# Kernel tuning notes

Measured on AMD Instinct MI355X. Metric: run time of the kernel, lower is better.

The kernel has to match this reference:

```python
import jax, jax.numpy as jnp
import numpy as np

B, F, T, D = 8, 256, 32, 1024
NEG = -1e30


def setup_inputs() -> dict:
    key = jax.random.key(0)
    ks = jax.random.split(key, 10)
    s = 1.0 / np.sqrt(D)
    return {
        "features": jax.random.normal(ks[0], (B, F, D), jnp.float32),
        "masks": jnp.ones((B, F), jnp.float32),  # unused by the module
        "textual_features": jax.random.normal(ks[1], (B, T, D), jnp.float32),
        "q_masks": jax.random.randint(ks[2], (B, T), 0, 2, jnp.int32),
        "Ws": jax.random.normal(ks[3], (D, D), jnp.float32) * s,
        "W": jax.random.normal(ks[4], (D, D), jnp.float32) * s,
        "w": jax.random.normal(ks[5], (D, 1), jnp.float32) * s,
        "b": jax.random.normal(ks[6], (1, D), jnp.float32) * s,
        "Wcw": jax.random.normal(ks[7], (1, D), jnp.float32) * s,
        "bcw": jnp.zeros((1,), jnp.float32),
        "Wcb": jax.random.normal(ks[8], (1, D), jnp.float32) * s,
        "bcb": jnp.zeros((1,), jnp.float32),
    }


def reference(features, masks, textual_features, q_masks, Ws, W, w, b, Wcw, bcw, Wcb, bcb):
    # Vectorized over all f_len frames at once (original loops over k).
    txt_proj = jnp.einsum("btd,de->bte", textual_features, Ws)   # [B,T,D]
    feat_proj = jnp.einsum("bfd,de->bfe", features, W)           # [B,F,D]
    # additive-attention hidden: [B,F,T,D]
    h = jnp.tanh(txt_proj[:, None, :, :] + feat_proj[:, :, None, :] + b[None, None, :, :][..., 0, :])
    rho = jnp.einsum("bftd,d->bft", h, w[:, 0])                  # [B,F,T]
    qm = q_masks.astype(jnp.float32)
    rho = rho + (1.0 - qm)[:, None, :] * NEG                     # mask_logits
    att = jax.nn.softmax(rho, axis=-1)                          # over t_len
    txt_h = jnp.einsum("bft,btd->bfd", att, textual_features)    # [B,F,D]
    w_s = jnp.tanh(jnp.einsum("bfd,od->bfo", txt_h, Wcw) + bcw)  # [B,F,1]
    b_s = jnp.tanh(jnp.einsum("bfd,od->bfo", txt_h, Wcb) + bcb)  # [B,F,1]
    return w_s * features + b_s
```

## Files before the change

### kernel.cpp

```cpp
#include <hip/hip_runtime.h>
#include <math.h>

#define Bdim 8
#define Fdim 256
#define Tdim 32
#define Ddim 1024
#define NEGV (-1e30f)
#define TANH_SCALE 2.8853900817779268f
#define LOG2E 1.4426950408889634f

typedef unsigned short ushort;
using short8  = __attribute__((ext_vector_type(8))) short;
using floatx4 = __attribute__((ext_vector_type(4))) float;

__device__ __forceinline__ float fexp2(float x) { return __builtin_amdgcn_exp2f(x); }
__device__ __forceinline__ float frcp(float x)  { return __builtin_amdgcn_rcpf(x); }

__device__ __forceinline__ float fast_tanh(float x) {
    return 1.0f - 2.0f * frcp(fexp2(x * TANH_SCALE) + 1.0f);
}

__device__ __forceinline__ ushort f2bf(float f) {
    unsigned u = __float_as_uint(f);
    unsigned r = u + 0x7FFFu + ((u >> 16) & 1u);
    return (ushort)(r >> 16);
}

__global__ __launch_bounds__(256) void prep(
    const float* __restrict__ feat, const float* __restrict__ txt,
    const float* __restrict__ W, const float* __restrict__ Ws,
    ushort* __restrict__ featB, ushort* __restrict__ txtB,
    ushort* __restrict__ WtB, ushort* __restrict__ WstB)
{
    __shared__ ushort tile[32][33];
    const int blk = blockIdx.x;
    const int NCAST = Bdim * Fdim + Bdim * Tdim;
    if (blk < NCAST) {
        const float* in; ushort* out; int base;
        if (blk < Bdim * Fdim) { in = feat; out = featB; base = blk * Ddim; }
        else { in = txt; out = txtB; base = (blk - Bdim * Fdim) * Ddim; }
        const int i = base + threadIdx.x * 4;
        float4 v = *(const float4*)(in + i);
        ushort4 o;
        o.x = f2bf(v.x); o.y = f2bf(v.y); o.z = f2bf(v.z); o.w = f2bf(v.w);
        *(ushort4*)(out + i) = o;
    } else {
        int t = blk - NCAST;
        const float* in = (t < 1024) ? W : Ws;
        ushort* out = (t < 1024) ? WtB : WstB;
        t &= 1023;
        const int bx = (t & 31) * 32;
        const int by = (t >> 5) * 32;
        const int tx = threadIdx.x & 31;
        const int tg = threadIdx.x >> 5;
        #pragma unroll
        for (int r = tg; r < 32; r += 8)
            tile[r][tx] = f2bf(in[(size_t)(by + r) * Ddim + bx + tx]);
        __syncthreads();
        #pragma unroll
        for (int r = tg; r < 32; r += 8)
            out[(size_t)(bx + r) * Ddim + by + tx] = tile[tx][r];
    }
}

#define GBK 32

__device__ __forceinline__ int swz(int row, int kUsh) {
    int ch = (kUsh >> 3) ^ ((row >> 1) & 3);
    return row * GBK + ch * 8 + (kUsh & 7);
}

__global__ __launch_bounds__(256) void gemm_dual(
    const ushort* __restrict__ A1, const ushort* __restrict__ Bt1, float* __restrict__ C1,
    const ushort* __restrict__ A2, const ushort* __restrict__ Bt2, float* __restrict__ C2,
    const float* __restrict__ bias2)
{
    const int K = Ddim, N = Ddim;
    const int by = blockIdx.y;
    const ushort* A; const ushort* Bt; float* C; const float* bias; int m0;
    if (by < 32) { A = A1; Bt = Bt1; C = C1; bias = nullptr; m0 = by * 64; }
    else         { A = A2; Bt = Bt2; C = C2; bias = bias2;  m0 = (by - 32) * 64; }
    const int n0 = blockIdx.x * 64;

    __shared__ __align__(16) ushort As[64 * GBK];
    __shared__ __align__(16) ushort Bs[64 * GBK];

    const int tid  = threadIdx.x;
    const int l    = tid & 63;
    const int wave = tid >> 6;

    const int srow = tid >> 2;
    const int scol = (tid & 3) * 8;

    const int wm = (wave >> 1) * 32;
    const int wn = (wave & 1) * 32;

    floatx4 acc[2][2];
    #pragma unroll
    for (int i = 0; i < 2; ++i)
        #pragma unroll
        for (int j = 0; j < 2; ++j)
            acc[i][j] = (floatx4){0.0f, 0.0f, 0.0f, 0.0f};

    const int lm = l & 15;
    const int lk = (l >> 4) * 8;

    const ushort* aptr = A  + (size_t)(m0 + srow) * K + scol;
    const ushort* bptr = Bt + (size_t)(n0 + srow) * K + scol;

    uint4 av = *(const uint4*)(aptr);
    uint4 bv = *(const uint4*)(bptr);

    for (int k0 = 0; k0 < K; k0 += GBK) {
        __syncthreads();
        *(uint4*)&As[swz(srow, scol)] = av;
        *(uint4*)&Bs[swz(srow, scol)] = bv;
        __syncthreads();

        int kn = k0 + GBK; if (kn >= K) kn = 0;
        av = *(const uint4*)(aptr + kn);
        bv = *(const uint4*)(bptr + kn);

        short8 af0 = *(const short8*)&As[swz(wm + lm,      lk)];
        short8 af1 = *(const short8*)&As[swz(wm + 16 + lm, lk)];
        short8 bf0 = *(const short8*)&Bs[swz(wn + lm,      lk)];
        short8 bf1 = *(const short8*)&Bs[swz(wn + 16 + lm, lk)];
        acc[0][0] = __builtin_amdgcn_mfma_f32_16x16x32_bf16(af0, bf0, acc[0][0], 0, 0, 0);
        acc[0][1] = __builtin_amdgcn_mfma_f32_16x16x32_bf16(af0, bf1, acc[0][1], 0, 0, 0);
        acc[1][0] = __builtin_amdgcn_mfma_f32_16x16x32_bf16(af1, bf0, acc[1][0], 0, 0, 0);
        acc[1][1] = __builtin_amdgcn_mfma_f32_16x16x32_bf16(af1, bf1, acc[1][1], 0, 0, 0);
    }

    const int rowq = (l >> 4) * 4;
    #pragma unroll
    for (int im = 0; im < 2; ++im) {
        #pragma unroll
        for (int in_ = 0; in_ < 2; ++in_) {
            const int col = n0 + wn + in_ * 16 + lm;
            float badd = (bias != nullptr) ? bias[col] : 0.0f;
            #pragma unroll
            for (int r = 0; r < 4; ++r) {
                const int row = m0 + wm + im * 16 + rowq + r;
                C[(size_t)row * N + col] = (acc[im][in_][r] + badd) * TANH_SCALE;
            }
        }
    }
}

__global__ __launch_bounds__(256, 4) void attn_fused(
    const float* __restrict__ feat,
    const float* __restrict__ txt,
    const int*   __restrict__ qmask,
    const float* __restrict__ fp_s,
    const float* __restrict__ tp_s,
    const float* __restrict__ wvec,
    const float* __restrict__ Wcw,
    const float* __restrict__ bcw,
    const float* __restrict__ Wcb,
    const float* __restrict__ bcb,
    float* __restrict__ out)
{
    const int blk  = blockIdx.x;
    const int f0   = blk * 2;
    const int b    = f0 >> 8;
    const int tid  = threadIdx.x;
    const int lane = tid & 63;
    const int wave = tid >> 6;

    __shared__ float srho[2][Tdim];
    __shared__ float satt[2][Tdim];
    __shared__ float sred[4][4];

    float4 wv[4], fva[4], fvb[4];
    const float* fr0 = fp_s + (size_t)f0 * Ddim;
    const float* fr1 = fr0 + Ddim;
    #pragma unroll
    for (int it = 0; it < 4; ++it) {
        const int d = lane * 4 + it * 256;
        wv[it]  = *(const float4*)&wvec[d];
        fva[it] = *(const float4*)&fr0[d];
        fvb[it] = *(const float4*)&fr1[d];
    }
    float sumw = 0.0f;
    #pragma unroll
    for (int it = 0; it < 4; ++it)
        sumw += wv[it].x + wv[it].y + wv[it].z + wv[it].w;
    #pragma unroll
    for (int off = 32; off; off >>= 1) sumw += __shfl_xor(sumw, off, 64);

    const float* tpb = tp_s + (size_t)b * Tdim * Ddim;
    for (int tt = 0; tt < 8; ++tt) {
        const int t = wave * 8 + tt;
        const float* tr = tpb + (size_t)t * Ddim;
        float s0a = 0.0f, s0b = 0.0f, s1a = 0.0f, s1b = 0.0f;
        #pragma unroll
        for (int it = 0; it < 4; ++it) {
            const int d = lane * 4 + it * 256;
            float4 tv = *(const float4*)&tr[d];
            float e, r;
            e = fexp2(tv.x + fva[it].x); r = frcp(e + 1.0f); s0a = fmaf(wv[it].x, r, s0a);
            e = fexp2(tv.y + fva[it].y); r = frcp(e + 1.0f); s0b = fmaf(wv[it].y, r, s0b);
            e = fexp2(tv.z + fva[it].z); r = frcp(e + 1.0f); s0a = fmaf(wv[it].z, r, s0a);
            e = fexp2(tv.w + fva[it].w); r = frcp(e + 1.0f); s0b = fmaf(wv[it].w, r, s0b);
            e = fexp2(tv.x + fvb[it].x); r = frcp(e + 1.0f); s1a = fmaf(wv[it].x, r, s1a);
            e = fexp2(tv.y + fvb[it].y); r = frcp(e + 1.0f); s1b = fmaf(wv[it].y, r, s1b);
            e = fexp2(tv.z + fvb[it].z); r = frcp(e + 1.0f); s1a = fmaf(wv[it].z, r, s1a);
            e = fexp2(tv.w + fvb[it].w); r = frcp(e + 1.0f); s1b = fmaf(wv[it].w, r, s1b);
        }
        float s0 = s0a + s0b, s1 = s1a + s1b;
        #pragma unroll
        for (int off = 32; off; off >>= 1) {
            s0 += __shfl_xor(s0, off, 64);
            s1 += __shfl_xor(s1, off, 64);
        }
        if (lane == 0) { srho[0][t] = s0; srho[1][t] = s1; }
    }
    __syncthreads();

    if (wave == 0) {
        const int f = lane >> 5, t = lane & 31;
        const float q = (float)qmask[b * Tdim + t];
        float L = sumw - 2.0f * srho[f][t] + (1.0f - q) * NEGV;
        float m = L;
        #pragma unroll
        for (int off = 16; off; off >>= 1) m = fmaxf(m, __shfl_xor(m, off, 64));
        float e = fexp2((L - m) * LOG2E);
        float ssum = e;
        #pragma unroll
        for (int off = 16; off; off >>= 1) ssum += __shfl_xor(ssum, off, 64);
        satt[f][t] = e * frcp(ssum);
    }
    __syncthreads();

    const float* txtb = txt + (size_t)b * Tdim * Ddim;
    const int d0 = tid * 4;
    float4 th0 = {0,0,0,0}, th1 = {0,0,0,0};
    #pragma unroll 8
    for (int t = 0; t < Tdim; ++t) {
        float4 tv = *(const float4*)&txtb[(size_t)t * Ddim + d0];
        const float a0 = satt[0][t], a1 = satt[1][t];
        th0.x = fmaf(a0, tv.x, th0.x); th0.y = fmaf(a0, tv.y, th0.y);
        th0.z = fmaf(a0, tv.z, th0.z); th0.w = fmaf(a0, tv.w, th0.w);
        th1.x = fmaf(a1, tv.x, th1.x); th1.y = fmaf(a1, tv.y, th1.y);
        th1.z = fmaf(a1, tv.z, th1.z); th1.w = fmaf(a1, tv.w, th1.w);
    }

    float4 wcw = *(const float4*)&Wcw[d0];
    float4 wcb = *(const float4*)&Wcb[d0];
    float p00 = th0.x*wcw.x + th0.y*wcw.y + th0.z*wcw.z + th0.w*wcw.w;
    float p01 = th0.x*wcb.x + th0.y*wcb.y + th0.z*wcb.z + th0.w*wcb.w;
    float p10 = th1.x*wcw.x + th1.y*wcw.y + th1.z*wcw.z + th1.w*wcw.w;
    float p11 = th1.x*wcb.x + th1.y*wcb.y + th1.z*wcb.z + th1.w*wcb.w;
    #pragma unroll
    for (int off = 32; off; off >>= 1) {
        p00 += __shfl_xor(p00, off, 64);
        p01 += __shfl_xor(p01, off, 64);
        p10 += __shfl_xor(p10, off, 64);
        p11 += __shfl_xor(p11, off, 64);
    }
    if (lane == 0) {
        sred[wave][0] = p00; sred[wave][1] = p01;
        sred[wave][2] = p10; sred[wave][3] = p11;
    }
    __syncthreads();
    const float c00 = sred[0][0] + sred[1][0] + sred[2][0] + sred[3][0];
    const float c01 = sred[0][1] + sred[1][1] + sred[2][1] + sred[3][1];
    const float c10 = sred[0][2] + sred[1][2] + sred[2][2] + sred[3][2];
    const float c11 = sred[0][3] + sred[1][3] + sred[2][3] + sred[3][3];
    const float ws0 = fast_tanh(c00 + bcw[0]);
    const float bs0 = fast_tanh(c01 + bcb[0]);
    const float ws1 = fast_tanh(c10 + bcw[0]);
    const float bs1 = fast_tanh(c11 + bcb[0]);

    const float* ft0 = feat + (size_t)f0 * Ddim;
    float4 v0 = *(const float4*)&ft0[d0];
    float4 v1 = *(const float4*)&ft0[Ddim + d0];
    float4 o0, o1;
    o0.x = fmaf(ws0, v0.x, bs0); o0.y = fmaf(ws0, v0.y, bs0);
    o0.z = fmaf(ws0, v0.z, bs0); o0.w = fmaf(ws0, v0.w, bs0);
    o1.x = fmaf(ws1, v1.x, bs1); o1.y = fmaf(ws1, v1.y, bs1);
    o1.z = fmaf(ws1, v1.z, bs1); o1.w = fmaf(ws1, v1.w, bs1);
    *(float4*)&out[(size_t)f0 * Ddim + d0] = o0;
    *(float4*)&out[(size_t)f0 * Ddim + Ddim + d0] = o1;
}

extern "C" void kernel_launch(void* const* d_in, const int* in_sizes, int n_in,
                              void* d_out, int out_size, void* d_ws, size_t ws_size,
                              hipStream_t stream) {
    const float* features = (const float*)d_in[0];
    const float* textual  = (const float*)d_in[2];
    const int*   q_masks  = (const int*)d_in[3];
    const float* Ws       = (const float*)d_in[4];
    const float* W        = (const float*)d_in[5];
    const float* wvec     = (const float*)d_in[6];
    const float* bvec     = (const float*)d_in[7];
    const float* Wcw      = (const float*)d_in[8];
    const float* bcw      = (const float*)d_in[9];
    const float* Wcb      = (const float*)d_in[10];
    const float* bcb      = (const float*)d_in[11];
    float* out = (float*)d_out;

    float*  fp_ws = (float*)d_ws;
    float*  tp_ws = fp_ws + (size_t)Bdim * Fdim * Ddim;
    ushort* featB = (ushort*)(tp_ws + (size_t)Bdim * Tdim * Ddim);
    ushort* txtB  = featB + (size_t)Bdim * Fdim * Ddim;
    ushort* WtB   = txtB + (size_t)Bdim * Tdim * Ddim;
    ushort* WstB  = WtB + (size_t)Ddim * Ddim;

    prep<<<Bdim * Fdim + Bdim * Tdim + 2048, 256, 0, stream>>>(
        features, textual, W, Ws, featB, txtB, WtB, WstB);
    gemm_dual<<<dim3(16, 36), 256, 0, stream>>>(
        featB, WtB, fp_ws, txtB, WstB, tp_ws, bvec);
    attn_fused<<<(Bdim * Fdim) / 2, 256, 0, stream>>>(
        features, textual, q_masks, fp_ws, tp_ws,
        wvec, Wcw, bcw, Wcb, bcb, out);
}
```

Baseline: 128.2 us.

## Enlarge GEMM tile to 128x64 and stage operands via direct global-to-LDS loads

The dual projection GEMM now uses 128x64 output tiles, so each wave computes a 64x32 sub-tile with eight MFMAs per k-step. Operand tiles are copied straight from global memory into LDS with global_load_lds, replacing the register-staged copy and the XOR swizzle. The aim is more operand reuse per LDS load and fewer VGPR round-trips. In exchange it drops the register prefetch of the next k-slice, may bring back LDS bank conflicts without the swizzle, and halves the grid to 288 blocks.

```diff
diff --git a/kernel.cpp b/kernel.cpp
--- a/kernel.cpp
+++ b/kernel.cpp
@@ -25,6 +25,10 @@
     unsigned r = u + 0x7FFFu + ((u >> 16) & 1u);
     return (ushort)(r >> 16);
 }
+
+#define GLOAD_LDS16(gp, lp) __builtin_amdgcn_global_load_lds(                   \
+    (const __attribute__((address_space(1))) void*)(gp),                        \
+    (__attribute__((address_space(3))) void*)(lp), 16, 0, 0)
 
 __global__ __launch_bounds__(256) void prep(
     const float* __restrict__ feat, const float* __restrict__ txt,
@@ -63,12 +67,9 @@
     }
 }
 
+#define GBM 128
+#define GBN 64
 #define GBK 32
-
-__device__ __forceinline__ int swz(int row, int kUsh) {
-    int ch = (kUsh >> 3) ^ ((row >> 1) & 3);
-    return row * GBK + ch * 8 + (kUsh & 7);
-}
 
 __global__ __launch_bounds__(256) void gemm_dual(
     const ushort* __restrict__ A1, const ushort* __restrict__ Bt1, float* __restrict__ C1,
@@ -78,26 +79,26 @@
     const int K = Ddim, N = Ddim;
     const int by = blockIdx.y;
     const ushort* A; const ushort* Bt; float* C; const float* bias; int m0;
-    if (by < 32) { A = A1; Bt = Bt1; C = C1; bias = nullptr; m0 = by * 64; }
-    else         { A = A2; Bt = Bt2; C = C2; bias = bias2;  m0 = (by - 32) * 64; }
-    const int n0 = blockIdx.x * 64;
-
-    __shared__ __align__(16) ushort As[64 * GBK];
-    __shared__ __align__(16) ushort Bs[64 * GBK];
+    if (by < 16) { A = A1; Bt = Bt1; C = C1; bias = nullptr; m0 = by * GBM; }
+    else         { A = A2; Bt = Bt2; C = C2; bias = bias2;  m0 = (by - 16) * GBM; }
+    const int n0 = blockIdx.x * GBN;
+
+    __shared__ __align__(16) ushort As[GBM * GBK];
+    __shared__ __align__(16) ushort Bs[GBN * GBK];
 
     const int tid  = threadIdx.x;
     const int l    = tid & 63;
     const int wave = tid >> 6;
 
-    const int srow = tid >> 2;
-    const int scol = (tid & 3) * 8;
-
-    const int wm = (wave >> 1) * 32;
+    const int crow = l >> 2;
+    const int ccol = (l & 3) * 8;
+
+    const int wm = (wave >> 1) * 64;
     const int wn = (wave & 1) * 32;
 
-    floatx4 acc[2][2];
-    #pragma unroll
-    for (int i = 0; i < 2; ++i)
+    floatx4 acc[4][2];
+    #pragma unroll
+    for (int i = 0; i < 4; ++i)
         #pragma unroll
         for (int j = 0; j < 2; ++j)
             acc[i][j] = (floatx4){0.0f, 0.0f, 0.0f, 0.0f};
@@ -105,35 +106,39 @@
     const int lm = l & 15;
     const int lk = (l >> 4) * 8;
 
-    const ushort* aptr = A  + (size_t)(m0 + srow) * K + scol;
-    const ushort* bptr = Bt + (size_t)(n0 + srow) * K + scol;
-
-    uint4 av = *(const uint4*)(aptr);
-    uint4 bv = *(const uint4*)(bptr);
+    const ushort* aSrc0 = A  + (size_t)(m0 + wave * 16       + crow) * K + ccol;
+    const ushort* aSrc1 = A  + (size_t)(m0 + (wave + 4) * 16 + crow) * K + ccol;
+    const ushort* bSrc  = Bt + (size_t)(n0 + wave * 16       + crow) * K + ccol;
+    ushort* aDst0 = &As[(wave * 16) * GBK];
+    ushort* aDst1 = &As[((wave + 4) * 16) * GBK];
+    ushort* bDst  = &Bs[(wave * 16) * GBK];
 
     for (int k0 = 0; k0 < K; k0 += GBK) {
         __syncthreads();
-        *(uint4*)&As[swz(srow, scol)] = av;
-        *(uint4*)&Bs[swz(srow, scol)] = bv;
+        GLOAD_LDS16(aSrc0 + k0, aDst0);
+        GLOAD_LDS16(aSrc1 + k0, aDst1);
+        GLOAD_LDS16(bSrc  + k0, bDst);
         __syncthreads();
 
-        int kn = k0 + GBK; if (kn >= K) kn = 0;
-        av = *(const uint4*)(aptr + kn);
-        bv = *(const uint4*)(bptr + kn);
-
-        short8 af0 = *(const short8*)&As[swz(wm + lm,      lk)];
-        short8 af1 = *(const short8*)&As[swz(wm + 16 + lm, lk)];
-        short8 bf0 = *(const short8*)&Bs[swz(wn + lm,      lk)];
-        short8 bf1 = *(const short8*)&Bs[swz(wn + 16 + lm, lk)];
+        short8 af0 = *(const short8*)&As[(wm +  0 + lm) * GBK + lk];
+        short8 af1 = *(const short8*)&As[(wm + 16 + lm) * GBK + lk];
+        short8 af2 = *(const short8*)&As[(wm + 32 + lm) * GBK + lk];
+        short8 af3 = *(const short8*)&As[(wm + 48 + lm) * GBK + lk];
+        short8 bf0 = *(const short8*)&Bs[(wn +  0 + lm) * GBK + lk];
+        short8 bf1 = *(const short8*)&Bs[(wn + 16 + lm) * GBK + lk];
         acc[0][0] = __builtin_amdgcn_mfma_f32_16x16x32_bf16(af0, bf0, acc[0][0], 0, 0, 0);
         acc[0][1] = __builtin_amdgcn_mfma_f32_16x16x32_bf16(af0, bf1, acc[0][1], 0, 0, 0);
         acc[1][0] = __builtin_amdgcn_mfma_f32_16x16x32_bf16(af1, bf0, acc[1][0], 0, 0, 0);
         acc[1][1] = __builtin_amdgcn_mfma_f32_16x16x32_bf16(af1, bf1, acc[1][1], 0, 0, 0);
+        acc[2][0] = __builtin_amdgcn_mfma_f32_16x16x32_bf16(af2, bf0, acc[2][0], 0, 0, 0);
+        acc[2][1] = __builtin_amdgcn_mfma_f32_16x16x32_bf16(af2, bf1, acc[2][1], 0, 0, 0);
+        acc[3][0] = __builtin_amdgcn_mfma_f32_16x16x32_bf16(af3, bf0, acc[3][0], 0, 0, 0);
+        acc[3][1] = __builtin_amdgcn_mfma_f32_16x16x32_bf16(af3, bf1, acc[3][1], 0, 0, 0);
     }
 
     const int rowq = (l >> 4) * 4;
     #pragma unroll
-    for (int im = 0; im < 2; ++im) {
+    for (int im = 0; im < 4; ++im) {
         #pragma unroll
         for (int in_ = 0; in_ < 2; ++in_) {
             const int col = n0 + wn + in_ * 16 + lm;
@@ -309,7 +314,7 @@
 
     prep<<<Bdim * Fdim + Bdim * Tdim + 2048, 256, 0, stream>>>(
         features, textual, W, Ws, featB, txtB, WtB, WstB);
-    gemm_dual<<<dim3(16, 36), 256, 0, stream>>>(
+    gemm_dual<<<dim3(Ddim / GBN, 18), 256, 0, stream>>>(
         featB, WtB, fp_ws, txtB, WstB, tp_ws, bvec);
     attn_fused<<<(Bdim * Fdim) / 2, 256, 0, stream>>>(
         features, textual, q_masks, fp_ws, tp_ws,
```

New measurement: 129.7 us. No clear change (+1.1%).
